# Kernel tuning notes

Hardware: AMD Instinct MI355X
Metric: run time of the kernel (lower is better)

Reference implementation:

```python
import jax, jax.numpy as jnp
import numpy as np

N, F, E = 2048, 4, 65536
D, H, FF = 256, 4, 2048  # d_model, n_heads, transformer feedforward dim
HD = D // H


def setup_inputs() -> dict:
    key = jax.random.key(0)
    ks = jax.random.split(key, 26)
    p = lambda k, shape, fan_in: (jax.random.normal(k, shape, jnp.float32) / np.sqrt(fan_in))
    return {
        "features": jax.random.normal(ks[0], (N, F), jnp.float32),
        "edges": jax.random.randint(ks[1], (2, E), 0, N, jnp.int64),
        # Embedder.linear: Linear(1, 256)
        "lin_w": p(ks[2], (D, 1), 1), "lin_b": jnp.zeros((D,), jnp.float32),
        # TransformerEncoderLayer self-attention
        "in_proj_w": p(ks[3], (3 * D, D), D), "in_proj_b": jnp.zeros((3 * D,), jnp.float32),
        "out_w": p(ks[4], (D, D), D), "out_b": jnp.zeros((D,), jnp.float32),
        "ln1_g": jnp.ones((D,), jnp.float32), "ln1_b": jnp.zeros((D,), jnp.float32),
        # feedforward
        "ffn_w1": p(ks[5], (FF, D), D), "ffn_b1": jnp.zeros((FF,), jnp.float32),
        "ffn_w2": p(ks[6], (D, FF), FF), "ffn_b2": jnp.zeros((D,), jnp.float32),
        "ln2_g": jnp.ones((D,), jnp.float32), "ln2_b": jnp.zeros((D,), jnp.float32),
        # 4 GCNConv layers (torch Linear convention: weight [out, in])
        "W1": p(ks[7], (512, D), D), "b1": jnp.zeros((512,), jnp.float32),
        "W2": p(ks[8], (512, 512), 512), "b2": jnp.zeros((512,), jnp.float32),
        "W3": p(ks[9], (512, 512), 512), "b3": jnp.zeros((512,), jnp.float32),
        "W4": p(ks[10], (512, 512), 512), "b4": jnp.zeros((512,), jnp.float32),
    }


def _layer_norm(x, g, b, eps=1e-5):
    m = jnp.mean(x, axis=-1, keepdims=True)
    v = jnp.mean((x - m) ** 2, axis=-1, keepdims=True)
    return (x - m) / jnp.sqrt(v + eps) * g + b


def _gcn_conv(x, W, b, src, dst, n):
    # PyG GCNConv: h = x @ W^T; add self-loops; norm = deg^-1/2[src]*deg^-1/2[dst];
    # out = scatter_add(norm * h[src] -> dst) + bias
    h = x @ W.T
    loop = jnp.arange(n, dtype=src.dtype)
    s = jnp.concatenate([src, loop])
    d = jnp.concatenate([dst, loop])
    deg = jax.ops.segment_sum(jnp.ones_like(d, dtype=h.dtype), d, num_segments=n)
    dinv = jnp.where(deg > 0, deg ** -0.5, 0.0)
    norm = dinv[s] * dinv[d]
    return jax.ops.segment_sum(h[s] * norm[:, None], d, num_segments=n) + b


def reference(features, edges, lin_w, lin_b, in_proj_w, in_proj_b, out_w, out_b,
              ln1_g, ln1_b, ffn_w1, ffn_b1, ffn_w2, ffn_b2, ln2_g, ln2_b,
              W1, b1, W2, b2, W3, b3, W4, b4):
    n, f = features.shape
    # Embedder: [N,F,1] -> Linear(1,D) -> [N,F,D]; seq-first transformer (seq=N, batch=F)
    x = features[..., None] @ lin_w.T + lin_b  # [N,F,D]
    qkv = x @ in_proj_w.T + in_proj_b          # [N,F,3D]
    q, k, v = jnp.split(qkv, 3, axis=-1)
    split = lambda t: t.reshape(n, f, H, HD).transpose(1, 2, 0, 3)  # [F,H,N,hd]
    q, k, v = split(q), split(k), split(v)
    scores = jnp.einsum('bhqd,bhkd->bhqk', q, k) / np.sqrt(HD)      # [F,H,N,N]
    attn = jax.nn.softmax(scores, axis=-1)
    o = jnp.einsum('bhqk,bhkd->bhqd', attn, v).transpose(2, 0, 1, 3).reshape(n, f, D)
    o = o @ out_w.T + out_b
    x = _layer_norm(x + o, ln1_g, ln1_b)
    ff = jax.nn.relu(x @ ffn_w1.T + ffn_b1) @ ffn_w2.T + ffn_b2
    x = _layer_norm(x + ff, ln2_g, ln2_b)
    x = jax.nn.relu(jnp.mean(x, axis=1))  # mean over feature-batch dim -> [N,D]

    src, dst = edges[0], edges[1]
    x = jax.nn.relu(_gcn_conv(x, W1, b1, src, dst, n))
    x = jax.nn.relu(_gcn_conv(x, W2, b2, src, dst, n))
    x = jax.nn.relu(_gcn_conv(x, W3, b3, src, dst, n))
    x = _gcn_conv(x, W4, b4, src, dst, n)
    return x
```

## Files before the change

kernel.cpp:

```cpp
#include <hip/hip_runtime.h>
#include <hip/hip_bf16.h>
#include <math.h>

#define NN   2048
#define FB   4
#define DD   256
#define EE   65536
#define NT   (NN*FB)
#define FFD  2048

typedef unsigned int u32;
typedef unsigned short u16;
typedef __attribute__((ext_vector_type(4))) float f32x4;
typedef __attribute__((ext_vector_type(8))) short bf16x8;

#define OFF_W2   0
#define OFF_G1   524288
#define OFF_G2   655360
#define OFF_G3   917504
#define OFF_G4   1179648
#define WBF_TOT  1441792

__device__ float g_A[768], g_B[768];
__device__ float g_coefA[4], g_coefC[4];
__device__ float g_meanv[6], g_G[36];
__device__ float g_Vx[8*DD];
__device__ u16   g_w1vh[FFD*8];
__device__ float g_m[NT*4];
__device__ float g_cc[NT*8];
__device__ u16   g_xmh[NN*DD];
__device__ u16   g_hsh[NN*512];
__device__ u16   g_xgh[NN*512];
__device__ u16   g_wbf[WBF_TOT];
__device__ __align__(64) int g_degp[NN*16];
__device__ __align__(64) int g_curp[NN*16];
__device__ int   g_off[NN+1], g_adj[EE];
__device__ float g_dinv[NN];

__device__ __forceinline__ u16 f2bf(float x) {
  u32 u = __float_as_uint(x);
  return (u16)((u + 0x7FFFu + ((u >> 16) & 1u)) >> 16);
}
__device__ __forceinline__ float bfl(u32 v) { return __uint_as_float(v << 16); }
__device__ __forceinline__ float bfh(u32 v) { return __uint_as_float(v & 0xffff0000u); }
__device__ __forceinline__ void gl_lds16(const void* g, void* l) {
  __builtin_amdgcn_global_load_lds(
      (const __attribute__((address_space(1))) u32*)g,
      (__attribute__((address_space(3))) u32*)l, 16, 0, 0);
}
__device__ __forceinline__ float qred(float v) {
  v += __shfl_xor(v, 1, 64);
  v += __shfl_xor(v, 2, 64);
  return v;
}
__device__ __forceinline__ void acc8(const uint4 v, float* a) {
  a[0]+=bfl(v.x); a[1]+=bfh(v.x);
  a[2]+=bfl(v.y); a[3]+=bfh(v.y);
  a[4]+=bfl(v.z); a[5]+=bfh(v.z);
  a[6]+=bfl(v.w); a[7]+=bfh(v.w);
}

__global__ __launch_bounds__(256) void k_fuse1(const float* __restrict__ ipw,
    const float* __restrict__ ipb, const float* __restrict__ linw,
    const float* __restrict__ linb) {
  __shared__ __align__(16) float sm[512];
  const int b = blockIdx.x, t = threadIdx.x;
  if (b < 12) {
    float* lw = sm; float* lb = sm + 256;
    lw[t] = linw[t]; lb[t] = linb[t];
    __syncthreads();
    int j = b*64 + (t>>2), c = t&3;
    const float4* row = (const float4*)&ipw[j*256 + c*64];
    float a = 0.f, bb = 0.f;
    #pragma unroll
    for (int q = 0; q < 16; q++) {
      float4 v = row[q]; int d0 = c*64 + q*4;
      a  += v.x*lw[d0] + v.y*lw[d0+1] + v.z*lw[d0+2] + v.w*lw[d0+3];
      bb += v.x*lb[d0] + v.y*lb[d0+1] + v.z*lb[d0+2] + v.w*lb[d0+3];
    }
    a = qred(a); bb = qred(bb);
    if (c == 0) { g_A[j] = a; g_B[j] = bb + ipb[j]; }
  } else {
    int i = (b - 12)*256 + t;
    if (i < NN*16) { g_degp[i] = 0; g_curp[i] = 0; }
  }
}

__global__ __launch_bounds__(256) void k_fuse2(const float* __restrict__ outw,
    const float* __restrict__ outb, const float* __restrict__ linw,
    const float* __restrict__ linb, const float* __restrict__ g1,
    const float* __restrict__ b1ln, const int* __restrict__ edges) {
  __shared__ __align__(16) float sm[512 + 4*27];
  const int b = blockIdx.x, t = threadIdx.x;
  if (b == 0) {
    int lane = t & 63, w = t >> 6;
    {
      float aq = g_A[w*64 + lane], ak = g_A[256 + w*64 + lane], bq = g_B[w*64 + lane];
      float pa = aq * ak, pc = bq * ak;
      #pragma unroll
      for (int o = 32; o > 0; o >>= 1) { pa += __shfl_down(pa, o, 64); pc += __shfl_down(pc, o, 64); }
      if (lane == 0) { g_coefA[w] = pa * 0.125f; g_coefC[w] = pc * 0.125f; }
    }
    float* A2 = sm; float* B2 = sm + 256; float* wred = sm + 512;
    A2[t] = g_A[512 + t]; B2[t] = g_B[512 + t];
    __syncthreads();
    const int d = t;
    const float4* row = (const float4*)&outw[d*256];
    float pv[4] = {0,0,0,0}, q0 = 0.f;
    #pragma unroll 8
    for (int q = 0; q < 64; q++) {
      float4 v = row[q]; int e0 = q*4; int h = q >> 4;
      pv[h] += v.x*A2[e0] + v.y*A2[e0+1] + v.z*A2[e0+2] + v.w*A2[e0+3];
      q0    += v.x*B2[e0] + v.y*B2[e0+1] + v.z*B2[e0+2] + v.w*B2[e0+3];
    }
    q0 += outb[d];
    float c0 = linb[d] + q0;
    float Mv[6] = { linw[d], pv[0], pv[1], pv[2], pv[3], c0 };
    float vals[27];
    { int idx = 0;
      #pragma unroll
      for (int k = 0; k < 6; k++) vals[idx++] = Mv[k];
      #pragma unroll
      for (int k = 0; k < 6; k++)
        #pragma unroll
        for (int l = 0; l < 6; l++) if (l >= k) vals[idx++] = Mv[k]*Mv[l];
    }
    #pragma unroll
    for (int k2 = 0; k2 < 27; k2++) {
      float v = vals[k2];
      #pragma unroll
      for (int o = 32; o > 0; o >>= 1) v += __shfl_down(v, o, 64);
      if (lane == 0) wred[w*27 + k2] = v;
    }
    __syncthreads();
    if (t < 27) {
      float s = wred[t] + wred[27 + t] + wred[54 + t] + wred[81 + t];
      if (t < 6) g_meanv[t] = s * (1.f/256.f);
      else {
        int p = t - 6, k = 0;
        while (p >= 6 - k) { p -= 6 - k; k++; }
        int l = k + p;
        g_G[k*6+l] = s; g_G[l*6+k] = s;
      }
    }
    #pragma unroll
    for (int k = 0; k < 6; k++) g_Vx[k*256 + d] = Mv[k] * g1[d];
    g_Vx[6*256 + d] = g1[d];
    g_Vx[7*256 + d] = b1ln[d];
  } else {
    int e = (b - 1)*256 + t;
    atomicAdd(&g_degp[edges[EE + e] * 16], 1);
  }
}

__global__ __launch_bounds__(256) void k_fuse3(const float* __restrict__ feat,
    const float* __restrict__ w1, const float* __restrict__ fb1,
    const float* __restrict__ w2c, const float* __restrict__ W1c,
    const float* __restrict__ W2c, const float* __restrict__ W3c,
    const float* __restrict__ W4c) {
  __shared__ __align__(16) char smraw[34816];
  const int b = blockIdx.x, t = threadIdx.x;
  if (b < 512) {
    float* fs = (float*)smraw;
    float* ss = fs + 8192;
    float* ww = ss + 256;
    for (int i = t; i < 2048; i += 256) {
      const float4 v = *(const float4*)&feat[i*4];
      fs[0*2048+i] = v.x; fs[1*2048+i] = v.y; fs[2*2048+i] = v.z; fs[3*2048+i] = v.w;
    }
    __syncthreads();
    int tuple = b * 64 + (t >> 2);
    int c = t & 3;
    int h = tuple & 3, f = (tuple >> 2) & 3, n = tuple >> 4;
    float fi = fs[f*2048 + n];
    float tt = g_coefA[h] * fi + g_coefC[h];
    float s = 0.f, wsum = 0.f;
    int j0 = c * 512;
    for (int j = j0; j < j0 + 512; j++) {
      float fj = fs[f*2048 + j];
      float e = __expf(tt * fj);
      s += e; wsum += e * fj;
    }
    ss[(t>>2)*4 + c] = s; ww[(t>>2)*4 + c] = wsum;
    __syncthreads();
    if (c == 0) {
      float S = ss[(t>>2)*4] + ss[(t>>2)*4+1] + ss[(t>>2)*4+2] + ss[(t>>2)*4+3];
      float W = ww[(t>>2)*4] + ww[(t>>2)*4+1] + ww[(t>>2)*4+2] + ww[(t>>2)*4+3];
      g_m[tuple] = W / S;
    }
  } else if (b < 544) {
    float* vx = (float*)smraw;
    #pragma unroll
    for (int k = 0; k < 8; k++) vx[k*256 + t] = g_Vx[k*256 + t];
    __syncthreads();
    int j = (b - 512)*64 + (t>>2), c = t&3;
    const float4* row = (const float4*)&w1[j*256 + c*64];
    float acc[8] = {0,0,0,0,0,0,0,0};
    #pragma unroll
    for (int q = 0; q < 16; q++) {
      float4 v = row[q]; int d0 = c*64 + q*4;
      #pragma unroll
      for (int k = 0; k < 8; k++)
        acc[k] += v.x*vx[k*256+d0] + v.y*vx[k*256+d0+1]
                + v.z*vx[k*256+d0+2] + v.w*vx[k*256+d0+3];
    }
    #pragma unroll
    for (int k = 0; k < 8; k++) acc[k] = qred(acc[k]);
    if (c == 0) {
      acc[7] += fb1[j];
      uint4 r;
      r.x = ((u32)f2bf(acc[1])<<16) | f2bf(acc[0]);
      r.y = ((u32)f2bf(acc[3])<<16) | f2bf(acc[2]);
      r.z = ((u32)f2bf(acc[5])<<16) | f2bf(acc[4]);
      r.w = ((u32)f2bf(acc[7])<<16) | f2bf(acc[6]);
      *(uint4*)&g_w1vh[j*8] = r;
    }
  } else if (b == 544) {
    int* wt = (int*)smraw;
    int base = t * 8;
    int v[8], ex[8], sum = 0;
    #pragma unroll
    for (int i = 0; i < 8; i++) { ex[i] = sum; v[i] = g_degp[(base+i)*16]; sum += v[i]; }
    int lane = t & 63, w = t >> 6;
    int inc = sum;
    #pragma unroll
    for (int o = 1; o < 64; o <<= 1) { int x = __shfl_up(inc, o, 64); if (lane >= o) inc += x; }
    if (lane == 63) wt[w] = inc;
    __syncthreads();
    int wb = 0;
    for (int j = 0; j < w; j++) wb += wt[j];
    int excl = wb + inc - sum;
    #pragma unroll
    for (int i = 0; i < 8; i++) {
      g_off[base+i] = excl + ex[i];
      g_dinv[base+i] = rsqrtf((float)(v[i] + 1));
    }
    if (t == 255) g_off[NN] = wb + inc;
  } else {
    int i = ((b - 545)*256 + t) * 4;
    const float* src; int off;
    if (i < OFF_G1)      { src = w2c; off = OFF_W2; }
    else if (i < OFF_G2) { src = W1c; off = OFF_G1; }
    else if (i < OFF_G3) { src = W2c; off = OFF_G2; }
    else if (i < OFF_G4) { src = W3c; off = OFF_G3; }
    else                 { src = W4c; off = OFF_G4; }
    float4 v = *(const float4*)&src[i - off];
    ushort4 r;
    r.x = f2bf(v.x); r.y = f2bf(v.y); r.z = f2bf(v.z); r.w = f2bf(v.w);
    *(ushort4*)&g_wbf[i] = r;
  }
}

__global__ __launch_bounds__(256) void k_fuse4(const float* __restrict__ feat,
                                               const int* __restrict__ edges) {
  const int b = blockIdx.x, t = threadIdx.x;
  if (b < 32) {
    int tok = b * 256 + t;
    int n = tok >> 2, f = tok & 3;
    float fi = feat[n*4 + f];
    float u[6] = { fi, g_m[tok*4+0], g_m[tok*4+1], g_m[tok*4+2], g_m[tok*4+3], 1.f };
    float mu = 0.f;
    #pragma unroll
    for (int k = 0; k < 6; k++) mu += g_meanv[k] * u[k];
    float q = 0.f;
    for (int k = 0; k < 6; k++)
      for (int l = 0; l < 6; l++) q += u[k] * g_G[k*6+l] * u[l];
    q *= (1.f/256.f);
    float var = q - mu * mu;
    float s = rsqrtf(var + 1e-5f);
    float4 w0; w0.x = fi*s; w0.y = u[1]*s; w0.z = u[2]*s; w0.w = u[3]*s;
    float4 w1v; w1v.x = u[4]*s; w1v.y = s; w1v.z = -mu*s; w1v.w = 1.f;
    *(float4*)&g_cc[tok*8]     = w0;
    *(float4*)&g_cc[tok*8 + 4] = w1v;
  } else {
    int e = (b - 32)*256 + t;
    int s = edges[e], d = edges[EE + e];
    int pos = atomicAdd(&g_curp[d*16], 1);
    g_adj[g_off[d] + pos] = s;
  }
}

__global__ __launch_bounds__(256) void k_ffnln(const float* __restrict__ fb2,
    const float* __restrict__ ln2g, const float* __restrict__ ln2b) {
  __shared__ __align__(16) char smp[79872];
  u16*   Bsl  = (u16*)smp;
  u16*   w1s  = (u16*)(smp + 32768);
  u16*   Asl  = (u16*)(smp + 65536);
  float* ccs  = (float*)(smp + 67584);
  float* vxs  = (float*)(smp + 68096);
  float* fb2s = (float*)(smp + 76288);
  float* g2s  = (float*)(smp + 77312);
  float* b2s  = (float*)(smp + 78336);
  float* part = (float*)(smp + 79360);

  const int b = blockIdx.x, t = threadIdx.x;
  const int w = t >> 6, lane = t & 63, fr = lane & 15, gk = lane >> 4;
  const int tok0 = b * 16;

  for (int i = t; i < 2048; i += 256) vxs[i] = g_Vx[i];
  #pragma unroll
  for (int q = 0; q < 8; q++) {
    int jj = t + q*256;
    uint4 v = *(const uint4*)&g_w1vh[jj*8];
    int idx = (jj & ~7) | ((jj ^ (jj >> 3)) & 7);
    *(uint4*)&w1s[idx*8] = v;
  }
  if (t < 32)                     ((float4*)ccs)[t]       = ((const float4*)&g_cc[tok0*8])[t];
  else if (t >= 64 && t < 128)    ((float4*)fb2s)[t-64]   = ((const float4*)fb2)[t-64];
  else if (t >= 128 && t < 192)   ((float4*)g2s)[t-128]   = ((const float4*)ln2g)[t-128];
  else if (t >= 192)              ((float4*)b2s)[t-192]   = ((const float4*)ln2b)[t-192];
  __syncthreads();

  const int arow = t >> 3, asub = t & 7;
  float ac[8];
  if (t < 128) {
    #pragma unroll
    for (int k = 0; k < 8; k++) ac[k] = ccs[arow*8 + k];
  }

  f32x4 acc[4] = {};
  const u16* W2p = g_wbf + OFF_W2;
  for (int k0 = 0; k0 < FFD; k0 += 64) {
    #pragma unroll
    for (int c = 0; c < 8; c++) {
      int rr = (w << 6) + (c << 3) + (lane >> 3);
      int ks = (((lane & 7) ^ (rr & 7)) << 3);
      gl_lds16(W2p + (size_t)rr*FFD + k0 + ks, Bsl + (w << 12) + (c << 9));
    }
    if (t < 128) {
      float h[8];
      #pragma unroll
      for (int e2 = 0; e2 < 8; e2++) {
        int idx = (k0 + 8*asub) | (e2 ^ asub);
        uint4 wv = *(const uint4*)&w1s[idx*8];
        float s = ac[0]*bfl(wv.x) + ac[1]*bfh(wv.x)
                + ac[2]*bfl(wv.y) + ac[3]*bfh(wv.y)
                + ac[4]*bfl(wv.z) + ac[5]*bfh(wv.z)
                + ac[6]*bfl(wv.w) + ac[7]*bfh(wv.w);
        h[e2] = fmaxf(s, 0.f);
      }
      uint4 r;
      r.x = ((u32)f2bf(h[1])<<16) | f2bf(h[0]);
      r.y = ((u32)f2bf(h[3])<<16) | f2bf(h[2]);
      r.z = ((u32)f2bf(h[5])<<16) | f2bf(h[4]);
      r.w = ((u32)f2bf(h[7])<<16) | f2bf(h[6]);
      *(uint4*)&Asl[(arow << 6) + ((asub ^ (arow & 7)) << 3)] = r;
    }
    __syncthreads();
    bf16x8 af[2], bfv[4][2];
    #pragma unroll
    for (int kk = 0; kk < 2; kk++) {
      int q = (kk << 2) + gk;
      af[kk] = *(const bf16x8*)&Asl[(fr << 6) + ((q ^ (fr & 7)) << 3)];
    }
    #pragma unroll
    for (int nb = 0; nb < 4; nb++) {
      int col = w*64 + nb*16 + fr;
      #pragma unroll
      for (int kk = 0; kk < 2; kk++) {
        int q = (kk << 2) + gk;
        bfv[nb][kk] = *(const bf16x8*)&Bsl[(col << 6) + ((q ^ (col & 7)) << 3)];
      }
    }
    #pragma unroll
    for (int kk = 0; kk < 2; kk++)
      #pragma unroll
      for (int nb = 0; nb < 4; nb++)
        acc[nb] = __builtin_amdgcn_mfma_f32_16x16x32_bf16(af[kk], bfv[nb][kk], acc[nb], 0, 0, 0);
    __syncthreads();
  }

  #pragma unroll
  for (int nb = 0; nb < 4; nb++) {
    int col = w*64 + nb*16 + fr;
    float fb = fb2s[col];
    #pragma unroll
    for (int r = 0; r < 4; r++) {
      int row = gk*4 + r;
      float x1 = 0.f;
      #pragma unroll
      for (int k = 0; k < 8; k++) x1 += ccs[row*8 + k] * vxs[k*256 + col];
      acc[nb][r] += fb + x1;
    }
  }
  float s1[4] = {0,0,0,0}, s2v[4] = {0,0,0,0};
  #pragma unroll
  for (int r = 0; r < 4; r++)
    #pragma unroll
    for (int nb = 0; nb < 4; nb++) {
      float v = acc[nb][r];
      s1[r] += v; s2v[r] += v*v;
    }
  #pragma unroll
  for (int o = 1; o < 16; o <<= 1) {
    #pragma unroll
    for (int r = 0; r < 4; r++) {
      s1[r]  += __shfl_xor(s1[r],  o, 64);
      s2v[r] += __shfl_xor(s2v[r], o, 64);
    }
  }
  if (fr == 0) {
    #pragma unroll
    for (int r = 0; r < 4; r++) {
      int row = gk*4 + r;
      part[(w*16 + row)*2 + 0] = s1[r];
      part[(w*16 + row)*2 + 1] = s2v[r];
    }
  }
  __syncthreads();
  float mu[4], inv[4];
  #pragma unroll
  for (int r = 0; r < 4; r++) {
    int row = gk*4 + r;
    float S1 = 0.f, S2 = 0.f;
    #pragma unroll
    for (int wv = 0; wv < 4; wv++) {
      S1 += part[(wv*16 + row)*2 + 0];
      S2 += part[(wv*16 + row)*2 + 1];
    }
    float m = S1 * (1.f/256.f);
    mu[r] = m;
    inv[r] = rsqrtf(S2 * (1.f/256.f) - m*m + 1e-5f);
  }
  const int node = b*4 + gk;
  #pragma unroll
  for (int nb = 0; nb < 4; nb++) {
    int col = w*64 + nb*16 + fr;
    float g = g2s[col], bb = b2s[col];
    float m = 0.f;
    #pragma unroll
    for (int r = 0; r < 4; r++)
      m += (acc[nb][r] - mu[r]) * inv[r] * g + bb;
    g_xmh[node*256 + col] = f2bf(fmaxf(m * 0.25f, 0.f));
  }
}

template<int DO_ROWSCALE, int OUT_BF16, int HAS_BIAS>
__global__ __launch_bounds__(256) void k_mm64(
    const u16* __restrict__ A, const u16* __restrict__ Bm, void* __restrict__ Cv,
    int M, int N, int K,
    const float* __restrict__ rowscale, const float* __restrict__ bias)
{
  __shared__ u16 Asl[32*64];
  __shared__ u16 Bsl[64*64];
  const int t = threadIdx.x;
  const int w = t >> 6, lane = t & 63;
  const int bm = blockIdx.y * 32, bn = blockIdx.x * 64;
  const int wr = w >> 1, wc = w & 1;
  const int fr = lane & 15;
  const int gk = lane >> 4;
  f32x4 acc[2] = {};
  for (int k0 = 0; k0 < K; k0 += 64) {
    {
      int r = (w << 3) + (lane >> 3);
      int ks = (((lane & 7) ^ (r & 7)) << 3);
      gl_lds16(A + (size_t)(bm + r)*K + k0 + ks, Asl + (w << 9));
    }
    #pragma unroll
    for (int c = 0; c < 2; c++) {
      int r2 = (w << 4) + (c << 3) + (lane >> 3);
      int ks2 = (((lane & 7) ^ (r2 & 7)) << 3);
      gl_lds16(Bm + (size_t)(bn + r2)*K + k0 + ks2, Bsl + (w << 10) + (c << 9));
    }
    __syncthreads();
    bf16x8 af[2], bfv[2][2];
    #pragma unroll
    for (int kk = 0; kk < 2; kk++) {
      int q = (kk << 2) + gk;
      int row = wr*16 + fr;
      af[kk] = *(const bf16x8*)&Asl[(row << 6) + ((q ^ (row & 7)) << 3)];
    }
    #pragma unroll
    for (int nb = 0; nb < 2; nb++) {
      int col = wc*32 + nb*16 + fr;
      #pragma unroll
      for (int kk = 0; kk < 2; kk++) {
        int q = (kk << 2) + gk;
        bfv[nb][kk] = *(const bf16x8*)&Bsl[(col << 6) + ((q ^ (col & 7)) << 3)];
      }
    }
    #pragma unroll
    for (int kk = 0; kk < 2; kk++)
      #pragma unroll
      for (int nb = 0; nb < 2; nb++)
        acc[nb] = __builtin_amdgcn_mfma_f32_16x16x32_bf16(af[kk], bfv[nb][kk], acc[nb], 0, 0, 0);
    __syncthreads();
  }
  #pragma unroll
  for (int r = 0; r < 4; r++) {
    int row = bm + wr*16 + gk*4 + r;
    float rs = DO_ROWSCALE ? rowscale[row] : 1.f;
    #pragma unroll
    for (int nb = 0; nb < 2; nb++) {
      int col = bn + wc*32 + nb*16 + fr;
      float v = acc[nb][r];
      if (HAS_BIAS) v += bias[col];
      if (DO_ROWSCALE) v *= rs;
      if (OUT_BF16) ((u16*)Cv)[(size_t)row*N + col] = f2bf(v);
      else ((float*)Cv)[(size_t)row*N + col] = v;
    }
  }
}

template<int OUT_BF16, int DO_RELU>
__global__ __launch_bounds__(256) void k_agg(const float* __restrict__ bias,
                                             void* __restrict__ outv) {
  const int t = threadIdx.x, w = t >> 6, lane = t & 63;
  const int i = blockIdx.x*4 + w;
  const int d = lane * 8;
  const uint4* tbl = (const uint4*)g_hsh;
  float a[8] = {0,0,0,0,0,0,0,0};
  acc8(tbl[i*64 + lane], a);
  int e0 = g_off[i], e1 = g_off[i+1];
  int e = e0;
  for (; e + 4 <= e1; e += 4) {
    int s0 = g_adj[e+0], s1 = g_adj[e+1], s2 = g_adj[e+2], s3 = g_adj[e+3];
    uint4 v0 = tbl[s0*64 + lane];
    uint4 v1 = tbl[s1*64 + lane];
    uint4 v2 = tbl[s2*64 + lane];
    uint4 v3 = tbl[s3*64 + lane];
    acc8(v0, a); acc8(v1, a); acc8(v2, a); acc8(v3, a);
  }
  for (; e < e1; e++) acc8(tbl[g_adj[e]*64 + lane], a);
  float di = g_dinv[i];
  const float4 b0 = *(const float4*)&bias[d];
  const float4 b1 = *(const float4*)&bias[d+4];
  a[0]=di*a[0]+b0.x; a[1]=di*a[1]+b0.y; a[2]=di*a[2]+b0.z; a[3]=di*a[3]+b0.w;
  a[4]=di*a[4]+b1.x; a[5]=di*a[5]+b1.y; a[6]=di*a[6]+b1.z; a[7]=di*a[7]+b1.w;
  if (DO_RELU) {
    #pragma unroll
    for (int q = 0; q < 8; q++) a[q] = fmaxf(a[q], 0.f);
  }
  if (OUT_BF16) {
    uint4 r;
    r.x = ((u32)f2bf(a[1])<<16) | f2bf(a[0]);
    r.y = ((u32)f2bf(a[3])<<16) | f2bf(a[2]);
    r.z = ((u32)f2bf(a[5])<<16) | f2bf(a[4]);
    r.w = ((u32)f2bf(a[7])<<16) | f2bf(a[6]);
    *(uint4*)&((u16*)outv)[i*512 + d] = r;
  } else {
    float4 r0; r0.x=a[0]; r0.y=a[1]; r0.z=a[2]; r0.w=a[3];
    float4 r1; r1.x=a[4]; r1.y=a[5]; r1.z=a[6]; r1.w=a[7];
    *(float4*)&((float*)outv)[i*512 + d]     = r0;
    *(float4*)&((float*)outv)[i*512 + d + 4] = r1;
  }
}

static float* symf(const void* s) { void* p = nullptr; (void)hipGetSymbolAddress(&p, s); return (float*)p; }

extern "C" void kernel_launch(void* const* d_in, const int* in_sizes, int n_in,
                              void* d_out, int out_size, void* d_ws, size_t ws_size,
                              hipStream_t stream) {
  const float* feat = (const float*)d_in[0];
  const int*   edges= (const int*)  d_in[1];
  const float* linw = (const float*)d_in[2];
  const float* linb = (const float*)d_in[3];
  const float* ipw  = (const float*)d_in[4];
  const float* ipb  = (const float*)d_in[5];
  const float* outw = (const float*)d_in[6];
  const float* outb = (const float*)d_in[7];
  const float* ln1g = (const float*)d_in[8];
  const float* ln1b = (const float*)d_in[9];
  const float* fw1  = (const float*)d_in[10];
  const float* fb1  = (const float*)d_in[11];
  const float* fw2  = (const float*)d_in[12];
  const float* fb2  = (const float*)d_in[13];
  const float* ln2g = (const float*)d_in[14];
  const float* ln2b = (const float*)d_in[15];
  const float* W1g  = (const float*)d_in[16];
  const float* b1g  = (const float*)d_in[17];
  const float* W2g  = (const float*)d_in[18];
  const float* b2g  = (const float*)d_in[19];
  const float* W3g  = (const float*)d_in[20];
  const float* b3g  = (const float*)d_in[21];
  const float* W4g  = (const float*)d_in[22];
  const float* b4g  = (const float*)d_in[23];
  float* out = (float*)d_out;

  u16*   p_xmh = (u16*)symf(HIP_SYMBOL(g_xmh));
  u16*   p_hsh = (u16*)symf(HIP_SYMBOL(g_hsh));
  u16*   p_xgh = (u16*)symf(HIP_SYMBOL(g_xgh));
  u16*   p_wbf = (u16*)symf(HIP_SYMBOL(g_wbf));
  float* p_dinv= symf(HIP_SYMBOL(g_dinv));

  k_fuse1<<<140,  256, 0, stream>>>(ipw, ipb, linw, linb);
  k_fuse2<<<257,  256, 0, stream>>>(outw, outb, linw, linb, ln1g, ln1b, edges);
  k_fuse3<<<1953, 256, 0, stream>>>(feat, fw1, fb1, fw2, W1g, W2g, W3g, W4g);
  k_fuse4<<<288,  256, 0, stream>>>(feat, edges);

  k_ffnln<<<512, 256, 0, stream>>>(fb2, ln2g, ln2b);

  k_mm64<1,1,0><<<dim3(8, 64), 256, 0, stream>>>(
      p_xmh, p_wbf + OFF_G1, p_hsh, NN, 512, 256, p_dinv, nullptr);
  k_agg<1,1><<<NN/4, 256, 0, stream>>>(b1g, p_xgh);
  k_mm64<1,1,0><<<dim3(8, 64), 256, 0, stream>>>(
      p_xgh, p_wbf + OFF_G2, p_hsh, NN, 512, 512, p_dinv, nullptr);
  k_agg<1,1><<<NN/4, 256, 0, stream>>>(b2g, p_xgh);
  k_mm64<1,1,0><<<dim3(8, 64), 256, 0, stream>>>(
      p_xgh, p_wbf + OFF_G3, p_hsh, NN, 512, 512, p_dinv, nullptr);
  k_agg<1,1><<<NN/4, 256, 0, stream>>>(b3g, p_xgh);
  k_mm64<1,1,0><<<dim3(8, 64), 256, 0, stream>>>(
      p_xgh, p_wbf + OFF_G4, p_hsh, NN, 512, 512, p_dinv, nullptr);
  k_agg<0,0><<<NN/4, 256, 0, stream>>>(b4g, out);
}
```

Before: 180.3 us.

## Double K tile in FFN kernel and stream W1 slices per step

The fused FFN+LayerNorm kernel now uses a K tile of 128 instead of 64, which halves the number of loop iterations and barriers. Instead of preloading the whole W1 table into LDS, it double-buffers 128-row W1 slices with async global-to-LDS loads. All 256 threads now compute the hidden activations, where only 128 did before. The bias, LayerNorm params and Vx now come straight from global memory instead of LDS. Together this shrinks LDS use and prologue cost, with the risk of more global reads in the epilogue and added register pressure.

```diff
diff --git a/kernel.cpp b/kernel.cpp
--- a/kernel.cpp
+++ b/kernel.cpp
@@ -282,57 +282,60 @@
 
 __global__ __launch_bounds__(256) void k_ffnln(const float* __restrict__ fb2,
     const float* __restrict__ ln2g, const float* __restrict__ ln2b) {
-  __shared__ __align__(16) char smp[79872];
+  __shared__ __align__(16) char smp[74752];
   u16*   Bsl  = (u16*)smp;
-  u16*   w1s  = (u16*)(smp + 32768);
   u16*   Asl  = (u16*)(smp + 65536);
-  float* ccs  = (float*)(smp + 67584);
-  float* vxs  = (float*)(smp + 68096);
-  float* fb2s = (float*)(smp + 76288);
-  float* g2s  = (float*)(smp + 77312);
-  float* b2s  = (float*)(smp + 78336);
-  float* part = (float*)(smp + 79360);
+  u16*   w1sl = (u16*)(smp + 69632);
+  float* ccs  = (float*)(smp + 73728);
+  float* part = (float*)(smp + 74240);
 
   const int b = blockIdx.x, t = threadIdx.x;
   const int w = t >> 6, lane = t & 63, fr = lane & 15, gk = lane >> 4;
   const int tok0 = b * 16;
-
-  for (int i = t; i < 2048; i += 256) vxs[i] = g_Vx[i];
+  const u16* W2p = g_wbf + OFF_W2;
+
+  if (t < 32) ((float4*)ccs)[t] = ((const float4*)&g_cc[tok0*8])[t];
+  if (w == 1) {
+    #pragma unroll
+    for (int hh = 0; hh < 2; hh++) {
+      int p = hh*64 + lane;
+      int q = (p & ~7) | ((p ^ (p >> 3)) & 7);
+      gl_lds16(g_w1vh + (size_t)q*8, w1sl + (hh << 9));
+    }
+  }
+  __syncthreads();
+
+  const int arow = t >> 4, aslot = t & 15;
+  float ac[8];
   #pragma unroll
-  for (int q = 0; q < 8; q++) {
-    int jj = t + q*256;
-    uint4 v = *(const uint4*)&g_w1vh[jj*8];
-    int idx = (jj & ~7) | ((jj ^ (jj >> 3)) & 7);
-    *(uint4*)&w1s[idx*8] = v;
-  }
-  if (t < 32)                     ((float4*)ccs)[t]       = ((const float4*)&g_cc[tok0*8])[t];
-  else if (t >= 64 && t < 128)    ((float4*)fb2s)[t-64]   = ((const float4*)fb2)[t-64];
-  else if (t >= 128 && t < 192)   ((float4*)g2s)[t-128]   = ((const float4*)ln2g)[t-128];
-  else if (t >= 192)              ((float4*)b2s)[t-192]   = ((const float4*)ln2b)[t-192];
-  __syncthreads();
-
-  const int arow = t >> 3, asub = t & 7;
-  float ac[8];
-  if (t < 128) {
-    #pragma unroll
-    for (int k = 0; k < 8; k++) ac[k] = ccs[arow*8 + k];
-  }
+  for (int k = 0; k < 8; k++) ac[k] = ccs[arow*8 + k];
 
   f32x4 acc[4] = {};
-  const u16* W2p = g_wbf + OFF_W2;
-  for (int k0 = 0; k0 < FFD; k0 += 64) {
-    #pragma unroll
-    for (int c = 0; c < 8; c++) {
-      int rr = (w << 6) + (c << 3) + (lane >> 3);
-      int ks = (((lane & 7) ^ (rr & 7)) << 3);
-      gl_lds16(W2p + (size_t)rr*FFD + k0 + ks, Bsl + (w << 12) + (c << 9));
-    }
-    if (t < 128) {
+  for (int it = 0; it < 16; it++) {
+    const int k0 = it << 7;
+    const int cur = it & 1;
+    #pragma unroll
+    for (int c = 0; c < 16; c++) {
+      int col0 = (w << 6) + (c << 2);
+      int colL = col0 + (lane >> 4);
+      int p = lane & 15;
+      int q = (p & 8) | ((p ^ (colL & 7)) & 7);
+      gl_lds16(W2p + (size_t)colL*FFD + k0 + q*8, Bsl + (col0 << 7));
+    }
+    if (w == 1 && it < 15) {
+      #pragma unroll
+      for (int hh = 0; hh < 2; hh++) {
+        int p = hh*64 + lane;
+        int q = (p & ~7) | ((p ^ (p >> 3)) & 7);
+        gl_lds16(g_w1vh + (size_t)(k0 + 128 + q)*8, w1sl + ((cur ^ 1) << 10) + (hh << 9));
+      }
+    }
+    {
       float h[8];
       #pragma unroll
       for (int e2 = 0; e2 < 8; e2++) {
-        int idx = (k0 + 8*asub) | (e2 ^ asub);
-        uint4 wv = *(const uint4*)&w1s[idx*8];
+        int ph = aslot*8 + (e2 ^ (aslot & 7));
+        uint4 wv = *(const uint4*)&w1sl[(cur << 10) + ph*8];
         float s = ac[0]*bfl(wv.x) + ac[1]*bfh(wv.x)
                 + ac[2]*bfl(wv.y) + ac[3]*bfh(wv.y)
                 + ac[4]*bfl(wv.z) + ac[5]*bfh(wv.z)
@@ -344,42 +347,36 @@
       r.y = ((u32)f2bf(h[3])<<16) | f2bf(h[2]);
       r.z = ((u32)f2bf(h[5])<<16) | f2bf(h[4]);
       r.w = ((u32)f2bf(h[7])<<16) | f2bf(h[6]);
-      *(uint4*)&Asl[(arow << 6) + ((asub ^ (arow & 7)) << 3)] = r;
-    }
-    __syncthreads();
-    bf16x8 af[2], bfv[4][2];
-    #pragma unroll
-    for (int kk = 0; kk < 2; kk++) {
-      int q = (kk << 2) + gk;
-      af[kk] = *(const bf16x8*)&Asl[(fr << 6) + ((q ^ (fr & 7)) << 3)];
-    }
-    #pragma unroll
-    for (int nb = 0; nb < 4; nb++) {
-      int col = w*64 + nb*16 + fr;
-      #pragma unroll
-      for (int kk = 0; kk < 2; kk++) {
-        int q = (kk << 2) + gk;
-        bfv[nb][kk] = *(const bf16x8*)&Bsl[(col << 6) + ((q ^ (col & 7)) << 3)];
+      int ph = (aslot & 8) | ((aslot ^ (arow & 7)) & 7);
+      *(uint4*)&Asl[(arow << 7) + (ph << 3)] = r;
+    }
+    __syncthreads();
+    #pragma unroll
+    for (int kk = 0; kk < 4; kk++) {
+      int qa = (kk << 2) + gk;
+      int pa = (qa & 8) | ((qa ^ (fr & 7)) & 7);
+      bf16x8 af = *(const bf16x8*)&Asl[(fr << 7) + (pa << 3)];
+      #pragma unroll
+      for (int nb = 0; nb < 4; nb++) {
+        int col = (w << 6) + (nb << 4) + fr;
+        int pb = (qa & 8) | ((qa ^ (col & 7)) & 7);
+        bf16x8 bv = *(const bf16x8*)&Bsl[(col << 7) + (pb << 3)];
+        acc[nb] = __builtin_amdgcn_mfma_f32_16x16x32_bf16(af, bv, acc[nb], 0, 0, 0);
       }
     }
-    #pragma unroll
-    for (int kk = 0; kk < 2; kk++)
-      #pragma unroll
-      for (int nb = 0; nb < 4; nb++)
-        acc[nb] = __builtin_amdgcn_mfma_f32_16x16x32_bf16(af[kk], bfv[nb][kk], acc[nb], 0, 0, 0);
     __syncthreads();
   }
 
   #pragma unroll
   for (int nb = 0; nb < 4; nb++) {
-    int col = w*64 + nb*16 + fr;
-    float fb = fb2s[col];
+    int col = (w << 6) + (nb << 4) + fr;
+    float fb = fb2[col];
     #pragma unroll
     for (int r = 0; r < 4; r++) {
       int row = gk*4 + r;
       float x1 = 0.f;
       #pragma unroll
-      for (int k = 0; k < 8; k++) x1 += ccs[row*8 + k] * vxs[k*256 + col];
+      for (int k = 0; k < 8; k++) x1 += ccs[row*8 + k] * g_Vx[k*256 + col];
       acc[nb][r] += fb + x1;
     }
   }
@@ -425,8 +422,8 @@
   const int node = b*4 + gk;
   #pragma unroll
   for (int nb = 0; nb < 4; nb++) {
-    int col = w*64 + nb*16 + fr;
-    float g = g2s[col], bb = b2s[col];
+    int col = (w << 6) + (nb << 4) + fr;
+    float g = ln2g[col], bb = ln2b[col];
     float m = 0.f;
     #pragma unroll
     for (int r = 0; r < 4; r++)
```

Result: faster. 166.4 us (median of 2 runs) (-7.7%).

## Stream W1 slices per k-step into double-buffered LDS to cut shared memory

Applied to the files above, without the earlier changes.

The FFN+LayerNorm kernel stops preloading the full W1 table, Vx and the bias and gamma/beta vectors into shared memory. It streams a 64-row W1 slice per k-iteration into a double buffer using async global-to-LDS loads, and reads the epilogue constants straight from global memory. This cuts LDS use from about 78KB to about 37KB, which allows more blocks per CU and removes a large prologue copy. The cost is extra small loads inside the loop and uncached global reads in the epilogue.

```diff
diff --git a/kernel.cpp b/kernel.cpp
--- a/kernel.cpp
+++ b/kernel.cpp
@@ -282,33 +282,23 @@
 
 __global__ __launch_bounds__(256) void k_ffnln(const float* __restrict__ fb2,
     const float* __restrict__ ln2g, const float* __restrict__ ln2b) {
-  __shared__ __align__(16) char smp[79872];
+  __shared__ __align__(16) char smp[37888];
   u16*   Bsl  = (u16*)smp;
-  u16*   w1s  = (u16*)(smp + 32768);
-  u16*   Asl  = (u16*)(smp + 65536);
-  float* ccs  = (float*)(smp + 67584);
-  float* vxs  = (float*)(smp + 68096);
-  float* fb2s = (float*)(smp + 76288);
-  float* g2s  = (float*)(smp + 77312);
-  float* b2s  = (float*)(smp + 78336);
-  float* part = (float*)(smp + 79360);
+  u16*   Asl  = (u16*)(smp + 32768);
+  u16*   w1sl = (u16*)(smp + 34816);
+  float* ccs  = (float*)(smp + 36864);
+  float* part = (float*)(smp + 37376);
 
   const int b = blockIdx.x, t = threadIdx.x;
   const int w = t >> 6, lane = t & 63, fr = lane & 15, gk = lane >> 4;
   const int tok0 = b * 16;
-
-  for (int i = t; i < 2048; i += 256) vxs[i] = g_Vx[i];
-  #pragma unroll
-  for (int q = 0; q < 8; q++) {
-    int jj = t + q*256;
-    uint4 v = *(const uint4*)&g_w1vh[jj*8];
-    int idx = (jj & ~7) | ((jj ^ (jj >> 3)) & 7);
-    *(uint4*)&w1s[idx*8] = v;
-  }
-  if (t < 32)                     ((float4*)ccs)[t]       = ((const float4*)&g_cc[tok0*8])[t];
-  else if (t >= 64 && t < 128)    ((float4*)fb2s)[t-64]   = ((const float4*)fb2)[t-64];
-  else if (t >= 128 && t < 192)   ((float4*)g2s)[t-128]   = ((const float4*)ln2g)[t-128];
-  else if (t >= 192)              ((float4*)b2s)[t-192]   = ((const float4*)ln2b)[t-192];
+  const u16* W2p = g_wbf + OFF_W2;
+
+  if (t < 32) ((float4*)ccs)[t] = ((const float4*)&g_cc[tok0*8])[t];
+  if (w == 1) {
+    int q = (lane & ~7) | ((lane ^ (lane >> 3)) & 7);
+    gl_lds16(g_w1vh + (size_t)q*8, w1sl);
+  }
   __syncthreads();
 
   const int arow = t >> 3, asub = t & 7;
@@ -319,20 +309,25 @@
   }
 
   f32x4 acc[4] = {};
-  const u16* W2p = g_wbf + OFF_W2;
-  for (int k0 = 0; k0 < FFD; k0 += 64) {
+  for (int it = 0; it < 32; it++) {
+    const int k0 = it << 6;
+    const int cur = it & 1;
     #pragma unroll
     for (int c = 0; c < 8; c++) {
       int rr = (w << 6) + (c << 3) + (lane >> 3);
       int ks = (((lane & 7) ^ (rr & 7)) << 3);
       gl_lds16(W2p + (size_t)rr*FFD + k0 + ks, Bsl + (w << 12) + (c << 9));
     }
+    if (w == 1 && it < 31) {
+      int q = (lane & ~7) | ((lane ^ (lane >> 3)) & 7);
+      gl_lds16(g_w1vh + (size_t)(k0 + 64 + q)*8, w1sl + ((cur ^ 1) << 9));
+    }
     if (t < 128) {
       float h[8];
       #pragma unroll
       for (int e2 = 0; e2 < 8; e2++) {
-        int idx = (k0 + 8*asub) | (e2 ^ asub);
-        uint4 wv = *(const uint4*)&w1s[idx*8];
+        int idx = asub*8 + (e2 ^ asub);
+        uint4 wv = *(const uint4*)&w1sl[(cur << 9) + idx*8];
         float s = ac[0]*bfl(wv.x) + ac[1]*bfh(wv.x)
                 + ac[2]*bfl(wv.y) + ac[3]*bfh(wv.y)
                 + ac[4]*bfl(wv.z) + ac[5]*bfh(wv.z)
@@ -355,7 +350,7 @@
     }
     #pragma unroll
     for (int nb = 0; nb < 4; nb++) {
-      int col = w*64 + nb*16 + fr;
+      int col = (w << 6) + (nb << 4) + fr;
       #pragma unroll
       for (int kk = 0; kk < 2; kk++) {
         int q = (kk << 2) + gk;
@@ -372,14 +367,14 @@
 
   #pragma unroll
   for (int nb = 0; nb < 4; nb++) {
-    int col = w*64 + nb*16 + fr;
-    float fb = fb2s[col];
+    int col = (w << 6) + (nb << 4) + fr;
+    float fb = fb2[col];
     #pragma unroll
     for (int r = 0; r < 4; r++) {
       int row = gk*4 + r;
       float x1 = 0.f;
       #pragma unroll
-      for (int k = 0; k < 8; k++) x1 += ccs[row*8 + k] * vxs[k*256 + col];
+      for (int k = 0; k < 8; k++) x1 += ccs[row*8 + k] * g_Vx[k*256 + col];
       acc[nb][r] += fb + x1;
     }
   }
@@ -425,8 +420,8 @@
   const int node = b*4 + gk;
   #pragma unroll
   for (int nb = 0; nb < 4; nb++) {
-    int col = w*64 + nb*16 + fr;
-    float g = g2s[col], bb = b2s[col];
+    int col = (w << 6) + (nb << 4) + fr;
+    float g = ln2g[col], bb = ln2b[col];
     float m = 0.f;
     #pragma unroll
     for (int r = 0; r < 4; r++)
```

Result: no change. 180.1 us (-0.1%).
